# Optimization experiments

Measured on AMD Instinct MI355X. Metric: run time of the kernel, lower is better.

## Reference

```python
import jax, jax.numpy as jnp
import numpy as np

B, S, D = 8, 512, 384
VOCAB = 50257


def setup_inputs() -> dict:
    key = jax.random.key(0)
    ks = jax.random.split(key, 8)
    tokens = jax.random.randint(ks[0], (B, S), 0, VOCAB)
    dep_types = jax.random.randint(ks[1], (B, S), 0, 64)
    dep_heads = jax.random.randint(ks[2], (B, S), 0, S)
    tok_table = jax.random.normal(ks[3], (VOCAB, D), dtype=jnp.float32) * 0.02
    # composition bilinear: out[o] = x1 @ Wc[o] @ x2 + bc[o]
    Wc = jax.random.normal(ks[4], (D, D, D), dtype=jnp.float32) * (1.0 / np.sqrt(D))
    bc = jax.random.normal(ks[5], (D,), dtype=jnp.float32) * 0.01
    # reduction Linear(seq_len, 1): weight (1, S), bias (1,)
    Wr = jax.random.normal(ks[6], (1, S), dtype=jnp.float32) * (1.0 / np.sqrt(S))
    br = jax.random.normal(ks[7], (1,), dtype=jnp.float32) * 0.01
    return {"tokens": tokens, "dep_types": dep_types, "dep_heads": dep_heads,
            "tok_table": tok_table, "Wc": Wc, "bc": bc, "Wr": Wr, "br": br}


def _composition_block(tok, heads, Wc, bc, Wr, br):
    # Original math (with the dep_transform-overwrite bug preserved):
    #   dep = tanh(tok)                                   [B,S,D]
    #   expanded[b,s1,s2,:] = tok[b,s2,:]
    #   masked_dep[b,s1,s2,:] = dep[b,s2,:] * (heads[b,s2]==s1)
    #   comp[b,s1,s2,o] = tanh(bilinear(tok[b,s2], masked_dep[b,s1,s2]))[o]
    #   y[b,s1,o] = sum_s2 Wr[0,s2]*comp[b,s1,s2,o] + br[0]
    # Since masked_dep is zero unless heads[b,s2]==s1, bilinear reduces to
    # bias-only (t_off) off-tree and full value (t_on) on-tree -> O(S) scatter.
    dep = jnp.tanh(tok)
    u = jnp.einsum('bsd,ode,bse->bso', tok, Wc, dep)      # [B,S,D] full bilinear value
    t_on = jnp.tanh(u + bc)                               # [B,S,D]
    t_off = jnp.tanh(bc)                                  # [D]
    w = Wr[0]                                             # [S]
    base = t_off * jnp.sum(w) + br[0]                     # [D]
    contrib = (t_on - t_off) * w[None, :, None]           # [B,S,D]
    scat = jax.vmap(lambda h, c: jnp.zeros((S, D), dtype=tok.dtype).at[h].add(c))(heads, contrib)
    return scat + base[None, None, :]                     # [B,S,D]


def reference(tokens, dep_types, dep_heads, tok_table, Wc, bc, Wr, br):
    depth = 1
    tok = tok_table[tokens]                               # [B,S,D]
    # dep_types embedding is computed in the original but its result is
    # discarded inside the block (bug); it does not affect the output.
    for _ in range(depth):
        tok = _composition_block(tok, dep_heads, Wc, bc, Wr, br)
    out_mask = (dep_heads == 0)[:, :, None]               # [B,S,1]
    return tok * out_mask.astype(tok.dtype)
```

## Files before the change

kernel.cpp:

```cpp
#include <hip/hip_runtime.h>

#define BB 8
#define SS 512
#define DD 384
#define K2 (DD * DD)
#define LCH 16
#define OT 2
#define KCH 4
#define GROUPS (K2 / 4)
#define GPC (GROUPS / KCH)
#define NT 512
#define ITERS (GPC / NT)
#define MAXL_CAP 1024

#define WS_LIST_OFF 16
#define WS_U_OFF 16400

__global__ void flag_kernel(const int* __restrict__ heads, int* __restrict__ countp,
                            int* __restrict__ list, int maxl) {
    int b = blockIdx.x;
    int s2 = threadIdx.x;
    int h = heads[b * SS + s2];
    if (heads[b * SS + h] == 0) {
        int idx = atomicAdd(countp, 1);
        if (idx < maxl) list[idx] = b * SS + s2;
    }
}

__global__ __launch_bounds__(NT, 6) void bilinear_kernel(
    const float* __restrict__ Wc, const float* __restrict__ tok_table,
    const int* __restrict__ tokens, const int* __restrict__ list,
    const int* __restrict__ countp, float* __restrict__ u, int maxl) {
    __shared__ alignas(16) float tokS[LCH][DD];
    __shared__ alignas(16) float depS[LCH][DD];

    const int tid = threadIdx.x;
    const int o0 = blockIdx.x * OT;
    const int g0 = blockIdx.y * GPC;

    int total = *countp;
    if (total > maxl) total = maxl;

    for (int cb = 0; cb < total; cb += LCH) {
        for (int idx = tid; idx < LCH * DD; idx += NT) {
            int l = idx / DD;
            int i = idx - l * DD;
            float t = 0.f;
            if (cb + l < total) {
                int pos = list[cb + l];
                t = tok_table[(size_t)tokens[pos] * DD + i];
            }
            tokS[l][i] = t;
            depS[l][i] = tanhf(t);
        }
        __syncthreads();

        float acc[LCH][OT];
#pragma unroll
        for (int l = 0; l < LCH; ++l)
#pragma unroll
            for (int j = 0; j < OT; ++j) acc[l][j] = 0.f;

        const float* wbase = Wc + (size_t)o0 * K2;
        float4 wv0, wv1;
        {
            const float* wp = wbase + 4 * (size_t)(g0 + tid);
            wv0 = *(const float4*)wp;
            wv1 = *(const float4*)(wp + K2);
        }

#pragma unroll 1
        for (int it = 0; it < ITERS; ++it) {
            int gc = g0 + it * NT + tid;

            float4 nv0 = make_float4(0.f, 0.f, 0.f, 0.f), nv1 = nv0;
            if (it + 1 < ITERS) {
                const float* wp = wbase + 4 * (size_t)(gc + NT);
                nv0 = *(const float4*)wp;
                nv1 = *(const float4*)(wp + K2);
            }

            int d = gc / 96;
            int e4 = gc - d * 96;

#pragma unroll
            for (int l = 0; l < LCH; ++l) {
                float td = tokS[l][d];
                float4 dv = *(const float4*)(&depS[l][e4 * 4]);
                float px = td * dv.x, py = td * dv.y, pz = td * dv.z, pw = td * dv.w;
                acc[l][0] += px * wv0.x + py * wv0.y + pz * wv0.z + pw * wv0.w;
                acc[l][1] += px * wv1.x + py * wv1.y + pz * wv1.z + pw * wv1.w;
            }
            wv0 = nv0;
            wv1 = nv1;
        }

        int lane = tid & 63;
#pragma unroll
        for (int l = 0; l < LCH; ++l) {
            if (cb + l < total) {
#pragma unroll
                for (int j = 0; j < OT; ++j) {
                    float v = acc[l][j];
                    for (int off = 32; off > 0; off >>= 1) v += __shfl_down(v, off, 64);
                    if (lane == 0)
                        atomicAdd(&u[(size_t)(cb + l) * DD + o0 + j], v);
                }
            }
        }
        __syncthreads();
    }
}

__global__ __launch_bounds__(128) void finalize_kernel(
    const int* __restrict__ heads, const float* __restrict__ Wr,
    const float* __restrict__ bc, const float* __restrict__ br,
    const int* __restrict__ list, const int* __restrict__ countp,
    const float* __restrict__ u, float* __restrict__ out, int maxl) {
    int row = blockIdx.x;
    int tid = threadIdx.x;
    if (heads[row] != 0) {
        if (tid < DD / 4) {
            float4 z = make_float4(0.f, 0.f, 0.f, 0.f);
            ((float4*)(out + (size_t)row * DD))[tid] = z;
        }
        return;
    }
    int b = row >> 9;
    int s1 = row & 511;

    float sumw = 0.f;
    for (int s = 0; s < SS; ++s) sumw += Wr[s];
    float brv = br[0];

    int total = *countp;
    if (total > maxl) total = maxl;

    for (int o = tid; o < DD; o += 128) {
        float bco = bc[o];
        float t_off = tanhf(bco);
        float val = t_off * sumw + brv;
        for (int l = 0; l < total; ++l) {
            int pos = list[l];
            if ((pos >> 9) == b && heads[pos] == s1) {
                val += (tanhf(u[(size_t)l * DD + o] + bco) - t_off) * Wr[pos & 511];
            }
        }
        out[(size_t)row * DD + o] = val;
    }
}

extern "C" void kernel_launch(void* const* d_in, const int* in_sizes, int n_in,
                              void* d_out, int out_size, void* d_ws, size_t ws_size,
                              hipStream_t stream) {
    const int* tokens = (const int*)d_in[0];
    const int* heads = (const int*)d_in[2];
    const float* tok_table = (const float*)d_in[3];
    const float* Wc = (const float*)d_in[4];
    const float* bc = (const float*)d_in[5];
    const float* Wr = (const float*)d_in[6];
    const float* br = (const float*)d_in[7];
    float* out = (float*)d_out;

    char* ws = (char*)d_ws;
    int* countp = (int*)ws;
    int* list = (int*)(ws + WS_LIST_OFF);
    float* u = (float*)(ws + WS_U_OFF);

    long maxl_l = ((long)ws_size - WS_U_OFF) / (DD * 4);
    int maxl = maxl_l < 0 ? 0 : (maxl_l > MAXL_CAP ? MAXL_CAP : (int)maxl_l);

    hipMemsetAsync(d_ws, 0, (size_t)WS_U_OFF + (size_t)maxl * DD * 4, stream);

    flag_kernel<<<BB, SS, 0, stream>>>(heads, countp, list, maxl);
    bilinear_kernel<<<dim3(DD / OT, KCH), NT, 0, stream>>>(
        Wc, tok_table, tokens, list, countp, u, maxl);
    finalize_kernel<<<BB * SS, 128, 0, stream>>>(
        heads, Wr, bc, br, list, countp, u, out, maxl);
}
```

Baseline: 392.7 us.

## Widen bilinear output tile, skip empty list slots, restructure finalize per batch

The bilinear kernel now computes four output channels per block with 256 threads and an 8-way K split. Each activation loaded from shared memory is reused across more weight rows, and groups of four list entries beyond the valid count are skipped. The cross-lane reduction becomes a butterfly fold followed by a shared-memory combine across warps, which cuts shuffle and atomic traffic. Finalize runs one block per batch and writes only rows whose head is zero, with the output zeroed by a memset. The cost is higher register pressure, and the hit list is capped at 64 rows per batch.

```diff
diff --git a/kernel.cpp b/kernel.cpp
--- a/kernel.cpp
+++ b/kernel.cpp
@@ -5,11 +5,11 @@
 #define DD 384
 #define K2 (DD * DD)
 #define LCH 16
-#define OT 2
-#define KCH 4
+#define OT 4
+#define KCH 8
+#define NT 256
 #define GROUPS (K2 / 4)
 #define GPC (GROUPS / KCH)
-#define NT 512
 #define ITERS (GPC / NT)
 #define MAXL_CAP 1024
 
@@ -27,7 +27,18 @@
     }
 }
 
-__global__ __launch_bounds__(NT, 6) void bilinear_kernel(
+template <int HALF>
+__device__ __forceinline__ void fold_step(float* red, int lane) {
+#pragma unroll
+    for (int i = 0; i < HALF; ++i) {
+        float lo = red[i], hi = red[i + HALF];
+        float send = (lane & HALF) ? lo : hi;
+        float recv = __shfl_xor(send, HALF, 64);
+        red[i] = (lane & HALF) ? (hi + recv) : (lo + recv);
+    }
+}
+
+__global__ __launch_bounds__(NT, 3) void bilinear_kernel(
     const float* __restrict__ Wc, const float* __restrict__ tok_table,
     const int* __restrict__ tokens, const int* __restrict__ list,
     const int* __restrict__ countp, float* __restrict__ u, int maxl) {
@@ -35,6 +46,8 @@
     __shared__ alignas(16) float depS[LCH][DD];
 
     const int tid = threadIdx.x;
+    const int lane = tid & 63;
+    const int wid = tid >> 6;
     const int o0 = blockIdx.x * OT;
     const int g0 = blockIdx.y * GPC;
 
@@ -55,6 +68,8 @@
         }
         __syncthreads();
 
+        const int lmax = total - cb;
+
         float acc[LCH][OT];
 #pragma unroll
         for (int l = 0; l < LCH; ++l)
@@ -62,91 +77,123 @@
             for (int j = 0; j < OT; ++j) acc[l][j] = 0.f;
 
         const float* wbase = Wc + (size_t)o0 * K2;
-        float4 wv0, wv1;
+        float4 wv[OT], nv[OT];
         {
             const float* wp = wbase + 4 * (size_t)(g0 + tid);
-            wv0 = *(const float4*)wp;
-            wv1 = *(const float4*)(wp + K2);
+#pragma unroll
+            for (int r = 0; r < OT; ++r) wv[r] = *(const float4*)(wp + (size_t)r * K2);
         }
 
 #pragma unroll 1
         for (int it = 0; it < ITERS; ++it) {
             int gc = g0 + it * NT + tid;
 
-            float4 nv0 = make_float4(0.f, 0.f, 0.f, 0.f), nv1 = nv0;
+#pragma unroll
+            for (int r = 0; r < OT; ++r) nv[r] = make_float4(0.f, 0.f, 0.f, 0.f);
             if (it + 1 < ITERS) {
                 const float* wp = wbase + 4 * (size_t)(gc + NT);
-                nv0 = *(const float4*)wp;
-                nv1 = *(const float4*)(wp + K2);
+#pragma unroll
+                for (int r = 0; r < OT; ++r) nv[r] = *(const float4*)(wp + (size_t)r * K2);
             }
 
             int d = gc / 96;
             int e4 = gc - d * 96;
 
 #pragma unroll
-            for (int l = 0; l < LCH; ++l) {
-                float td = tokS[l][d];
-                float4 dv = *(const float4*)(&depS[l][e4 * 4]);
-                float px = td * dv.x, py = td * dv.y, pz = td * dv.z, pw = td * dv.w;
-                acc[l][0] += px * wv0.x + py * wv0.y + pz * wv0.z + pw * wv0.w;
-                acc[l][1] += px * wv1.x + py * wv1.y + pz * wv1.z + pw * wv1.w;
-            }
-            wv0 = nv0;
-            wv1 = nv1;
-        }
-
-        int lane = tid & 63;
-#pragma unroll
-        for (int l = 0; l < LCH; ++l) {
-            if (cb + l < total) {
-#pragma unroll
-                for (int j = 0; j < OT; ++j) {
-                    float v = acc[l][j];
-                    for (int off = 32; off > 0; off >>= 1) v += __shfl_down(v, off, 64);
-                    if (lane == 0)
-                        atomicAdd(&u[(size_t)(cb + l) * DD + o0 + j], v);
+            for (int l4 = 0; l4 < LCH / 4; ++l4) {
+                if (l4 * 4 < lmax) {
+#pragma unroll
+                    for (int li = 0; li < 4; ++li) {
+                        const int l = l4 * 4 + li;
+                        float td = tokS[l][d];
+                        float4 dv = *(const float4*)(&depS[l][e4 * 4]);
+                        float px = td * dv.x, py = td * dv.y;
+                        float pz = td * dv.z, pw = td * dv.w;
+#pragma unroll
+                        for (int r = 0; r < OT; ++r)
+                            acc[l][r] += px * wv[r].x + py * wv[r].y +
+                                         pz * wv[r].z + pw * wv[r].w;
+                    }
                 }
             }
-        }
-        __syncthreads();
-    }
-}
-
-__global__ __launch_bounds__(128) void finalize_kernel(
+#pragma unroll
+            for (int r = 0; r < OT; ++r) wv[r] = nv[r];
+        }
+
+        float red[LCH * OT];
+#pragma unroll
+        for (int k = 0; k < LCH * OT; ++k) red[k] = acc[k >> 2][k & 3];
+        fold_step<32>(red, lane);
+        fold_step<16>(red, lane);
+        fold_step<8>(red, lane);
+        fold_step<4>(red, lane);
+        fold_step<2>(red, lane);
+        fold_step<1>(red, lane);
+
+        __syncthreads();
+        float* redS = &tokS[0][0];
+        redS[wid * 64 + lane] = red[0];
+        __syncthreads();
+        if (tid < 64) {
+            int l = tid >> 2, j = tid & 3;
+            if (l < lmax) {
+                float s = redS[tid] + redS[64 + tid] + redS[128 + tid] + redS[192 + tid];
+                atomicAdd(&u[(size_t)(cb + l) * DD + o0 + j], s);
+            }
+        }
+        __syncthreads();
+    }
+}
+
+__global__ __launch_bounds__(SS) void finalize_kernel(
     const int* __restrict__ heads, const float* __restrict__ Wr,
     const float* __restrict__ bc, const float* __restrict__ br,
     const int* __restrict__ list, const int* __restrict__ countp,
     const float* __restrict__ u, float* __restrict__ out, int maxl) {
-    int row = blockIdx.x;
+    int b = blockIdx.x;
     int tid = threadIdx.x;
-    if (heads[row] != 0) {
-        if (tid < DD / 4) {
-            float4 z = make_float4(0.f, 0.f, 0.f, 0.f);
-            ((float4*)(out + (size_t)row * DD))[tid] = z;
-        }
-        return;
-    }
-    int b = row >> 9;
-    int s1 = row & 511;
+
+    __shared__ float wpart[SS / 64];
+    __shared__ int hitlist[64];
+    __shared__ int nh;
+    if (tid == 0) nh = 0;
+    __syncthreads();
+
+    float w = Wr[tid];
+#pragma unroll
+    for (int off = 32; off > 0; off >>= 1) w += __shfl_down(w, off, 64);
+    if ((tid & 63) == 0) wpart[tid >> 6] = w;
+
+    if (heads[b * SS + tid] == 0) {
+        int i = atomicAdd(&nh, 1);
+        if (i < 64) hitlist[i] = tid;
+    }
+    __syncthreads();
 
     float sumw = 0.f;
-    for (int s = 0; s < SS; ++s) sumw += Wr[s];
+#pragma unroll
+    for (int q = 0; q < SS / 64; ++q) sumw += wpart[q];
     float brv = br[0];
 
     int total = *countp;
     if (total > maxl) total = maxl;
-
-    for (int o = tid; o < DD; o += 128) {
-        float bco = bc[o];
-        float t_off = tanhf(bco);
-        float val = t_off * sumw + brv;
-        for (int l = 0; l < total; ++l) {
-            int pos = list[l];
-            if ((pos >> 9) == b && heads[pos] == s1) {
-                val += (tanhf(u[(size_t)l * DD + o] + bco) - t_off) * Wr[pos & 511];
-            }
-        }
-        out[(size_t)row * DD + o] = val;
+    int hn = nh;
+    if (hn > 64) hn = 64;
+
+    for (int i = 0; i < hn; ++i) {
+        int s1 = hitlist[i];
+        if (tid < DD) {
+            int o = tid;
+            float bco = bc[o];
+            float t_off = tanhf(bco);
+            float val = t_off * sumw + brv;
+            for (int l = 0; l < total; ++l) {
+                int pos = list[l];
+                if ((pos >> 9) == b && heads[pos] == s1)
+                    val += (tanhf(u[(size_t)l * DD + o] + bco) - t_off) * Wr[pos & 511];
+            }
+            out[(size_t)(b * SS + s1) * DD + o] = val;
+        }
     }
 }
 
@@ -171,10 +218,11 @@
     int maxl = maxl_l < 0 ? 0 : (maxl_l > MAXL_CAP ? MAXL_CAP : (int)maxl_l);
 
     hipMemsetAsync(d_ws, 0, (size_t)WS_U_OFF + (size_t)maxl * DD * 4, stream);
+    hipMemsetAsync(d_out, 0, (size_t)out_size, stream);
 
     flag_kernel<<<BB, SS, 0, stream>>>(heads, countp, list, maxl);
     bilinear_kernel<<<dim3(DD / OT, KCH), NT, 0, stream>>>(
         Wc, tok_table, tokens, list, countp, u, maxl);
-    finalize_kernel<<<BB * SS, 128, 0, stream>>>(
+    finalize_kernel<<<BB, SS, 0, stream>>>(
         heads, Wr, bc, br, list, countp, u, out, maxl);
 }
```

Measured after the change: 373.2 us. -5.0%, faster.
